# Optimization experiments

Hardware: AMD Instinct MI355X
Metric: run time of the kernel (lower is better)

The kernel has to match this reference:

```python
import jax, jax.numpy as jnp
import numpy as np

N_NODES = 100000
N_EDGES = 3200000
N_FEAT = 128
NUM_GRAPHS = 1024
NUM_CLASSES = 2


def glorot(key, shape):
    lim = np.sqrt(6.0 / (shape[0] + shape[1]))
    return jax.random.uniform(key, shape, jnp.float32, -lim, lim)


def setup_inputs() -> dict:
    key = jax.random.key(0)
    ks = jax.random.split(key, 12)
    x = jax.random.normal(ks[0], (N_NODES, N_FEAT), jnp.float32)
    edge_index = jax.random.randint(ks[1], (2, N_EDGES), 0, N_NODES, jnp.int64)
    batch = jnp.sort(jax.random.randint(ks[2], (N_NODES,), 0, NUM_GRAPHS, jnp.int64))
    return {
        "x": x,
        "edge_index": edge_index,
        "batch": batch,
        "W1": glorot(ks[3], (N_FEAT, 16)), "b1": jnp.zeros((16,), jnp.float32),
        "W2": glorot(ks[4], (16, 32)),     "b2": jnp.zeros((32,), jnp.float32),
        "W3": glorot(ks[5], (32, 64)),     "b3": jnp.zeros((64,), jnp.float32),
        "Wl1": glorot(ks[6], (64, 64)),    "bl1": jnp.zeros((64,), jnp.float32),
        "Wl2": glorot(ks[7], (64, NUM_CLASSES)), "bl2": jnp.zeros((NUM_CLASSES,), jnp.float32),
    }


def _gcn_norm(edge_index, n):
    # Add self-loops, then symmetric normalization D^-1/2 (A+I) D^-1/2
    loop = jnp.arange(n, dtype=edge_index.dtype)
    src = jnp.concatenate([edge_index[0], loop])
    dst = jnp.concatenate([edge_index[1], loop])
    deg = jax.ops.segment_sum(jnp.ones_like(dst, jnp.float32), dst, num_segments=n)
    dinv = jnp.where(deg > 0, jax.lax.rsqrt(deg), 0.0)
    norm = dinv[src] * dinv[dst]  # [E+N]
    return src, dst, norm


def _gcn_layer(h, W, b, src, dst, norm, n):
    h = h @ W                                  # linear first (PyG GCNConv order)
    msg = norm[:, None] * h[src]               # gather + scale
    out = jax.ops.segment_sum(msg, dst, num_segments=n) + b
    return jax.nn.relu(out)


def reference(x, edge_index, batch, W1, b1, W2, b2, W3, b3, Wl1, bl1, Wl2, bl2):
    n = x.shape[0]
    src, dst, norm = _gcn_norm(edge_index, n)
    h = _gcn_layer(x, W1, b1, src, dst, norm, n)
    h = _gcn_layer(h, W2, b2, src, dst, norm, n)
    h = _gcn_layer(h, W3, b3, src, dst, norm, n)
    # global mean pool over graphs
    sums = jax.ops.segment_sum(h, batch, num_segments=NUM_GRAPHS)
    cnts = jax.ops.segment_sum(jnp.ones((n,), jnp.float32), batch, num_segments=NUM_GRAPHS)
    pooled = sums / jnp.maximum(cnts, 1.0)[:, None]
    # MLP head (sigmoid self.out is defined but never applied in forward)
    hid = jax.nn.relu(pooled @ Wl1 + bl1)
    return hid @ Wl2 + bl2
```

## Files before the change

kernel.cpp:

```cpp
#include <hip/hip_runtime.h>
#include <hip/hip_fp16.h>


constexpr int EPA1 = 8192;
constexpr int NPSB = 256;
constexpr int PAD1 = 400;

__device__ __forceinline__ void acc8(float4& A, float4& B, uint4 u) {
    __half2* ph = reinterpret_cast<__half2*>(&u);
    float2 f0 = __half22float2(ph[0]);
    float2 f1 = __half22float2(ph[1]);
    float2 f2 = __half22float2(ph[2]);
    float2 f3 = __half22float2(ph[3]);
    A.x += f0.x; A.y += f0.y; A.z += f1.x; A.w += f1.y;
    B.x += f2.x; B.y += f2.y; B.z += f3.x; B.w += f3.y;
}
__device__ __forceinline__ uint4 pack8(const float* h) {
    __half2 a = __floats2half2_rn(h[0], h[1]);
    __half2 b = __floats2half2_rn(h[2], h[3]);
    __half2 c = __floats2half2_rn(h[4], h[5]);
    __half2 d = __floats2half2_rn(h[6], h[7]);
    uint4 u;
    u.x = *reinterpret_cast<unsigned*>(&a);
    u.y = *reinterpret_cast<unsigned*>(&b);
    u.z = *reinterpret_cast<unsigned*>(&c);
    u.w = *reinterpret_cast<unsigned*>(&d);
    return u;
}

__global__ __launch_bounds__(1024) void k_hist1(const int* __restrict__ dst,
        int* __restrict__ cnt1, int nE, int NSB) {
    __shared__ int hist[512];
    int t = threadIdx.x;
    if (t < 512) hist[t] = 0;
    __syncthreads();
    int base = blockIdx.x * EPA1, end = min(base + EPA1, nE);
    for (int e = base + t; e < end; e += 1024)
        atomicAdd(&hist[dst[e] >> 8], 1);
    __syncthreads();
    if (t < NSB) cnt1[blockIdx.x * PAD1 + t] = hist[t];
}

__global__ __launch_bounds__(512) void k_scan1(const int* __restrict__ cnt1,
        int* __restrict__ po1, int* __restrict__ totals, int NBLK1) {
    __shared__ int sc[512];
    int sb = blockIdx.x, t = threadIdx.x;
    int v = (t < NBLK1) ? cnt1[t * PAD1 + sb] : 0;
    sc[t] = v;
    __syncthreads();
    for (int off = 1; off < 512; off <<= 1) {
        int u = (t >= off) ? sc[t - off] : 0;
        __syncthreads();
        sc[t] += u;
        __syncthreads();
    }
    if (t < NBLK1) po1[t * PAD1 + sb] = sc[t] - v;
    if (t == 511) totals[sb] = sc[511];
}

__global__ __launch_bounds__(1024) void k_scat1(const int* __restrict__ src,
        const int* __restrict__ dst, const int* __restrict__ po1,
        const int* __restrict__ totals, unsigned* __restrict__ ebuf,
        int nE, int NSB) {
    __shared__ int sc[512], cur[512];
    int t = threadIdx.x, blk = blockIdx.x;
    if (t < 512) sc[t] = (t < NSB) ? totals[t] : 0;
    __syncthreads();
    for (int off = 1; off < 512; off <<= 1) {
        int u = (t >= off && t < 512) ? sc[t - off] : 0;
        __syncthreads();
        if (t < 512) sc[t] += u;
        __syncthreads();
    }
    if (t < NSB) cur[t] = (sc[t] - totals[t]) + po1[blk * PAD1 + t];
    __syncthreads();
    int base = blk * EPA1, end = min(base + EPA1, nE);
    for (int e = base + t; e < end; e += 1024) {
        int s = src[e], d = dst[e];
        int pos = atomicAdd(&cur[d >> 8], 1);
        ebuf[pos] = ((unsigned)(d & 255) << 17) | (unsigned)s;
    }
}

__global__ __launch_bounds__(512) void k_sort2(const unsigned* __restrict__ ebuf,
        const int* __restrict__ totals, int* __restrict__ col,
        int* __restrict__ start, float* __restrict__ dinv,
        unsigned* __restrict__ poff, int n, int qsz, int NSB) {
    __shared__ int sc[512];
    __shared__ int hist4[1024], cur4[1024], excl[256];
    int b = blockIdx.x, t = threadIdx.x;
    sc[t] = (t < NSB) ? totals[t] : 0;
    __syncthreads();
    for (int off = 1; off < 512; off <<= 1) {
        int u = (t >= off) ? sc[t - off] : 0;
        __syncthreads();
        sc[t] += u;
        __syncthreads();
    }
    int eend = sc[b], ebase = eend - totals[b];
    hist4[t] = 0; hist4[t + 512] = 0;
    __syncthreads();
    for (int e = ebase + t; e < eend; e += 512) {
        unsigned u = ebuf[e];
        atomicAdd(&hist4[(u >> 17) * 4 + (int)(u & 0x1FFFFu) / qsz], 1);
    }
    __syncthreads();
    int c0 = 0, c1 = 0, c2 = 0, c3 = 0, v = 0;
    if (t < 256) {
        c0 = hist4[t * 4];     c1 = hist4[t * 4 + 1];
        c2 = hist4[t * 4 + 2]; c3 = hist4[t * 4 + 3];
        v = c0 + c1 + c2 + c3;
        excl[t] = v;
    }
    __syncthreads();
    for (int off = 1; off < 256; off <<= 1) {
        int u = (t >= off && t < 256) ? excl[t - off] : 0;
        __syncthreads();
        if (t < 256) excl[t] += u;
        __syncthreads();
    }
    if (t < 256) {
        int sbase = ebase + excl[t] - v;
        cur4[t * 4]     = sbase;
        cur4[t * 4 + 1] = sbase + c0;
        cur4[t * 4 + 2] = sbase + c0 + c1;
        cur4[t * 4 + 3] = sbase + c0 + c1 + c2;
        int node = (b << 8) + t;
        if (node < n) {
            start[node] = sbase;
            dinv[node] = rsqrtf((float)(v + 1));
            poff[node] = (unsigned)c0 | ((unsigned)c1 << 8) |
                         ((unsigned)c2 << 16) | ((unsigned)c3 << 24);
        }
    }
    __syncthreads();
    for (int e = ebase + t; e < eend; e += 512) {
        unsigned u = ebuf[e];
        int s = (int)(u & 0x1FFFFu);
        int pos = atomicAdd(&cur4[(u >> 17) * 4 + s / qsz], 1);
        col[pos] = s;
    }
}

template <int U4PR>
__device__ __forceinline__ void agg_gather8(const uint4* __restrict__ T,
        const int* __restrict__ col, int base, unsigned pk, int q,
        size_t selfIdx, float4& A, float4& B) {
    A = make_float4(0.f, 0.f, 0.f, 0.f);
    B = make_float4(0.f, 0.f, 0.f, 0.f);
    acc8(A, B, T[selfIdx]);
    #pragma unroll
    for (int p = 0; p < 4; ++p) {
        int len = (int)((pk >> (8 * p)) & 255u);
        int k = 0;
        for (; k + 4 <= len; k += 4) {
            uint4 u0 = T[(size_t)col[base + k]     * U4PR + q];
            uint4 u1 = T[(size_t)col[base + k + 1] * U4PR + q];
            uint4 u2 = T[(size_t)col[base + k + 2] * U4PR + q];
            uint4 u3 = T[(size_t)col[base + k + 3] * U4PR + q];
            acc8(A, B, u0); acc8(A, B, u1); acc8(A, B, u2); acc8(A, B, u3);
        }
        for (; k < len; ++k)
            acc8(A, B, T[(size_t)col[base + k] * U4PR + q]);
        base += len;
    }
}

__global__ void k_aggf16(const uint4* __restrict__ T, const int* __restrict__ start,
        const unsigned* __restrict__ poff, const int* __restrict__ col,
        const float* __restrict__ dinv, const float* __restrict__ bias,
        uint4* __restrict__ out, int n) {
    int idx = blockIdx.x * blockDim.x + threadIdx.x;
    int i = idx / 2, q = idx % 2;
    if (i >= n) return;
    float4 A, B;
    agg_gather8<2>(T, col, start[i], poff[i], q, (size_t)i * 2 + q, A, B);
    float d = dinv[i];
    float4 bA = ((const float4*)bias)[q * 2];
    float4 bB = ((const float4*)bias)[q * 2 + 1];
    float h[8];
    h[0] = d * fmaxf(d * A.x + bA.x, 0.0f);
    h[1] = d * fmaxf(d * A.y + bA.y, 0.0f);
    h[2] = d * fmaxf(d * A.z + bA.z, 0.0f);
    h[3] = d * fmaxf(d * A.w + bA.w, 0.0f);
    h[4] = d * fmaxf(d * B.x + bB.x, 0.0f);
    h[5] = d * fmaxf(d * B.y + bB.y, 0.0f);
    h[6] = d * fmaxf(d * B.z + bB.z, 0.0f);
    h[7] = d * fmaxf(d * B.w + bB.w, 0.0f);
    out[(size_t)i * 2 + q] = pack8(h);
}

__global__ __launch_bounds__(256) void k_aggf16_mm2(const uint4* __restrict__ T,
        const int* __restrict__ start, const unsigned* __restrict__ poff,
        const int* __restrict__ col, const float* __restrict__ dinv,
        const float* __restrict__ W2, const float* __restrict__ b2,
        uint4* __restrict__ out, int n) {
    __shared__ float sW[16 * 32];
    __shared__ float sB[32];
    int t = threadIdx.x;
    for (int j = t; j < 512; j += 256) sW[j] = W2[j];
    if (t < 32) sB[t] = b2[t];
    __syncthreads();
    int idx = blockIdx.x * blockDim.x + t;
    int i = idx / 2, q = idx % 2;
    if (i >= n) return;
    float4 A, B;
    agg_gather8<2>(T, col, start[i], poff[i], q, (size_t)i * 2 + q, A, B);
    float d = dinv[i];
    float a[8] = {d * A.x, d * A.y, d * A.z, d * A.w,
                  d * B.x, d * B.y, d * B.z, d * B.w};
    int lane = t & 63;
    int gbase = lane & ~1;
    float h[16];
    #pragma unroll
    for (int o = 0; o < 16; ++o) h[o] = sB[q * 16 + o];
    #pragma unroll
    for (int j = 0; j < 2; ++j) {
        #pragma unroll
        for (int kk = 0; kk < 8; ++kk) {
            float ak = __shfl(a[kk], gbase + j);
            const float* w0 = &sW[(j * 8 + kk) * 32 + q * 16];
            #pragma unroll
            for (int o = 0; o < 16; ++o) h[o] += ak * w0[o];
        }
    }
    float ho[16];
    #pragma unroll
    for (int o = 0; o < 16; ++o) ho[o] = d * fmaxf(h[o], 0.0f);
    out[(size_t)i * 4 + q * 2]     = pack8(ho);
    out[(size_t)i * 4 + q * 2 + 1] = pack8(ho + 8);
}

__global__ __launch_bounds__(512) void k_aggf32_mm3(const uint4* __restrict__ T,
        const int* __restrict__ start, const unsigned* __restrict__ poff,
        const int* __restrict__ col, const float* __restrict__ dinv,
        const float* __restrict__ W3, const float* __restrict__ b3,
        float* __restrict__ out, int n) {
    __shared__ float sW[32 * 64];
    __shared__ float sB[64];
    int t = threadIdx.x;
    for (int j = t; j < 2048; j += 512) sW[j] = W3[j];
    if (t < 64) sB[t] = b3[t];
    __syncthreads();
    int idx = blockIdx.x * blockDim.x + t;
    int i = idx / 4, q = idx % 4;
    if (i >= n) return;
    float4 A, B;
    agg_gather8<4>(T, col, start[i], poff[i], q, (size_t)i * 4 + q, A, B);
    float d = dinv[i];
    float a[8] = {d * A.x, d * A.y, d * A.z, d * A.w,
                  d * B.x, d * B.y, d * B.z, d * B.w};
    int lane = t & 63;
    int gbase = lane & ~3;
    float h[16];
    #pragma unroll
    for (int o = 0; o < 16; ++o) h[o] = sB[q * 16 + o];
    #pragma unroll
    for (int j = 0; j < 4; ++j) {
        #pragma unroll
        for (int kk = 0; kk < 8; ++kk) {
            float ak = __shfl(a[kk], gbase + j);
            const float* w0 = &sW[(j * 8 + kk) * 64 + q * 16];
            #pragma unroll
            for (int o = 0; o < 16; ++o) h[o] += ak * w0[o];
        }
    }
    float4* O4 = (float4*)out;
    float4 o0, o1, o2, o3;
    o0.x = fmaxf(h[0], 0.f);  o0.y = fmaxf(h[1], 0.f);
    o0.z = fmaxf(h[2], 0.f);  o0.w = fmaxf(h[3], 0.f);
    o1.x = fmaxf(h[4], 0.f);  o1.y = fmaxf(h[5], 0.f);
    o1.z = fmaxf(h[6], 0.f);  o1.w = fmaxf(h[7], 0.f);
    o2.x = fmaxf(h[8], 0.f);  o2.y = fmaxf(h[9], 0.f);
    o2.z = fmaxf(h[10], 0.f); o2.w = fmaxf(h[11], 0.f);
    o3.x = fmaxf(h[12], 0.f); o3.y = fmaxf(h[13], 0.f);
    o3.z = fmaxf(h[14], 0.f); o3.w = fmaxf(h[15], 0.f);
    size_t rb = (size_t)i * 16 + q * 4;
    O4[rb] = o0; O4[rb + 1] = o1; O4[rb + 2] = o2; O4[rb + 3] = o3;
}

__global__ __launch_bounds__(256) void k_mm1(const float4* __restrict__ X4,
        const float4* __restrict__ W4, const float* __restrict__ dinv,
        __half* __restrict__ out, int n) {
    __shared__ float4 xs[64 * 32];
    __shared__ float4 ws[512];
    int t = threadIdx.x;
    int nb = blockIdx.x * 64;
    ws[t] = W4[t]; ws[t + 256] = W4[t + 256];
    int lim = min(64, n - nb);
    #pragma unroll
    for (int it = 0; it < 8; ++it) {
        int idx = it * 256 + t;
        if ((idx >> 5) < lim) xs[idx] = X4[(size_t)nb * 32 + idx];
    }
    __syncthreads();
    int lane = t & 63, wv = t >> 6;
    int f = lane & 15, kc = lane >> 4;
    float wcol[32];
    #pragma unroll
    for (int kk = 0; kk < 32; ++kk)
        wcol[kk] = ((const float*)ws)[(kc * 32 + kk) * 16 + f];
    for (int ln = wv * 16; ln < wv * 16 + 16; ++ln) {
        if (ln >= lim) break;
        int i = nb + ln;
        float acc = 0.0f;
        #pragma unroll
        for (int j = 0; j < 8; ++j) {
            float4 hv = xs[ln * 32 + kc * 8 + j];
            acc += hv.x * wcol[4 * j]     + hv.y * wcol[4 * j + 1]
                 + hv.z * wcol[4 * j + 2] + hv.w * wcol[4 * j + 3];
        }
        acc += __shfl_xor(acc, 16);
        acc += __shfl_xor(acc, 32);
        if (kc == 0) out[(size_t)i * 16 + f] = __float2half_rn(acc * dinv[i]);
    }
}

__global__ __launch_bounds__(256) void k_poolhead(const float* __restrict__ h3,
        const int* __restrict__ batch, const float* __restrict__ Wl1,
        const float* __restrict__ bl1, const float* __restrict__ Wl2,
        const float* __restrict__ bl2, float* __restrict__ out, int n) {
    int g = blockIdx.x, t = threadIdx.x;
    int f = t & 63, r = t >> 6;
    __shared__ int sb[2];
    __shared__ float part[4][64];
    __shared__ float mean[64], hid[64];
    if (t < 2) {
        int target = g + t;
        int lo = 0, hi = n;
        while (lo < hi) {
            int mid = (lo + hi) >> 1;
            if (batch[mid] < target) lo = mid + 1; else hi = mid;
        }
        sb[t] = lo;
    }
    __syncthreads();
    int s = sb[0], e = sb[1];
    float acc = 0.0f;
    for (int i = s + r; i < e; i += 4) acc += h3[(size_t)i * 64 + f];
    part[r][f] = acc;
    __syncthreads();
    if (t < 64) {
        float c = fmaxf((float)(e - s), 1.0f);
        mean[t] = (part[0][t] + part[1][t] + part[2][t] + part[3][t]) / c;
    }
    __syncthreads();
    if (t < 64) {
        float a = bl1[t];
        #pragma unroll 8
        for (int k = 0; k < 64; ++k) a += mean[k] * Wl1[k * 64 + t];
        hid[t] = fmaxf(a, 0.0f);
    }
    __syncthreads();
    if (t < 2) {
        float o = bl2[t];
        #pragma unroll 8
        for (int k = 0; k < 64; ++k) o += hid[k] * Wl2[k * 2 + t];
        out[g * 2 + t] = o;
    }
}

extern "C" void kernel_launch(void* const* d_in, const int* in_sizes, int n_in,
                              void* d_out, int out_size, void* d_ws, size_t ws_size,
                              hipStream_t stream) {
    const float* x    = (const float*)d_in[0];
    const int*   ei   = (const int*)d_in[1];
    const int*   batch= (const int*)d_in[2];
    const float* W1   = (const float*)d_in[3];
    const float* b1   = (const float*)d_in[4];
    const float* W2   = (const float*)d_in[5];
    const float* b2   = (const float*)d_in[6];
    const float* W3   = (const float*)d_in[7];
    const float* b3   = (const float*)d_in[8];
    const float* Wl1  = (const float*)d_in[9];
    const float* bl1  = (const float*)d_in[10];
    const float* Wl2  = (const float*)d_in[11];
    const float* bl2  = (const float*)d_in[12];
    float* out = (float*)d_out;

    const int n  = in_sizes[2];
    const int nE = in_sizes[1] / 2;
    const int* src = ei;
    const int* dst = ei + nE;

    const int NSB   = (n + NPSB - 1) / NPSB;
    const int NBLK1 = (nE + EPA1 - 1) / EPA1;
    const int NG    = 1024;
    const int qsz   = (n + 3) / 4;

    char* w = (char*)d_ws;
    auto alloc_f = [&](size_t cnt) { float* p = (float*)w; w += cnt * 4; return p; };
    auto alloc_i = [&](size_t cnt) { int*   p = (int*)w;   w += cnt * 4; return p; };
    auto alloc_h = [&](size_t cnt) { __half* p = (__half*)w; w += cnt * 2; return p; };

    float*    dinv   = alloc_f(n);
    int*      start  = alloc_i(n);
    unsigned* poff   = (unsigned*)alloc_i(n);
    int*      cnt1   = alloc_i((size_t)NBLK1 * PAD1);
    int*      po1    = alloc_i((size_t)NBLK1 * PAD1);
    int*      totals = alloc_i(512);
    unsigned* ebuf   = (unsigned*)alloc_i(nE);
    int*      col    = alloc_i(nE);
    __half* Pd1 = alloc_h((size_t)n * 16);
    __half* h1d = alloc_h((size_t)n * 16);
    __half* h2d = alloc_h((size_t)n * 32);
    float*  h3  = alloc_f((size_t)n * 64);

    const int B = 256;
    auto g = [&](long long t) { return (int)((t + B - 1) / B); };

    k_hist1<<<NBLK1, 1024, 0, stream>>>(dst, cnt1, nE, NSB);
    k_scan1<<<NSB, 512, 0, stream>>>(cnt1, po1, totals, NBLK1);
    k_scat1<<<NBLK1, 1024, 0, stream>>>(src, dst, po1, totals, ebuf, nE, NSB);
    k_sort2<<<NSB, 512, 0, stream>>>(ebuf, totals, col, start, dinv, poff, n, qsz, NSB);

    k_mm1<<<(n + 63) / 64, 256, 0, stream>>>((const float4*)x, (const float4*)W1,
                                             dinv, Pd1, n);
    k_aggf16<<<g((long long)n * 2), B, 0, stream>>>((const uint4*)Pd1, start, poff,
                                                    col, dinv, b1, (uint4*)h1d, n);

    k_aggf16_mm2<<<g((long long)n * 2), B, 0, stream>>>((const uint4*)h1d, start,
                                                        poff, col, dinv, W2, b2,
                                                        (uint4*)h2d, n);

    k_aggf32_mm3<<<(int)(((long long)n * 4 + 511) / 512), 512, 0, stream>>>(
        (const uint4*)h2d, start, poff, col, dinv, W3, b3, h3, n);

    k_poolhead<<<NG, 256, 0, stream>>>(h3, batch, Wl1, bl1, Wl2, bl2, out, n);
}
```

Measured before the change: 202.2 us.

## Split each node's edge list across two thread halves in aggregation kernels

The three aggregation kernels now give each node twice as many threads. Each half gathers two of the four source-quartile segments, and the partial sums are combined with an xor shuffle. The fused matmuls are repartitioned so each thread produces 8 outputs instead of 16, which cuts per-thread register use and serial gather latency. Separately, the integer division by the quartile size in the sort kernel is replaced by a precomputed magic-number multiply-high. This doubles the thread count and adds shuffle traffic, and load imbalance between the two halves may waste lanes.

```diff
diff --git a/kernel.cpp b/kernel.cpp
--- a/kernel.cpp
+++ b/kernel.cpp
@@ -85,7 +85,7 @@
 __global__ __launch_bounds__(512) void k_sort2(const unsigned* __restrict__ ebuf,
         const int* __restrict__ totals, int* __restrict__ col,
         int* __restrict__ start, float* __restrict__ dinv,
-        unsigned* __restrict__ poff, int n, int qsz, int NSB) {
+        unsigned* __restrict__ poff, int n, unsigned qmagic, int NSB) {
     __shared__ int sc[512];
     __shared__ int hist4[1024], cur4[1024], excl[256];
     int b = blockIdx.x, t = threadIdx.x;
@@ -102,7 +102,8 @@
     __syncthreads();
     for (int e = ebase + t; e < eend; e += 512) {
         unsigned u = ebuf[e];
-        atomicAdd(&hist4[(u >> 17) * 4 + (int)(u & 0x1FFFFu) / qsz], 1);
+        unsigned s = u & 0x1FFFFu;
+        atomicAdd(&hist4[(u >> 17) * 4 + __umulhi(s, qmagic)], 1);
     }
     __syncthreads();
     int c0 = 0, c1 = 0, c2 = 0, c3 = 0, v = 0;
@@ -136,22 +137,19 @@
     __syncthreads();
     for (int e = ebase + t; e < eend; e += 512) {
         unsigned u = ebuf[e];
-        int s = (int)(u & 0x1FFFFu);
-        int pos = atomicAdd(&cur4[(u >> 17) * 4 + s / qsz], 1);
-        col[pos] = s;
+        unsigned s = u & 0x1FFFFu;
+        int pos = atomicAdd(&cur4[(u >> 17) * 4 + __umulhi(s, qmagic)], 1);
+        col[pos] = (int)s;
     }
 }
 
 template <int U4PR>
-__device__ __forceinline__ void agg_gather8(const uint4* __restrict__ T,
-        const int* __restrict__ col, int base, unsigned pk, int q,
-        size_t selfIdx, float4& A, float4& B) {
-    A = make_float4(0.f, 0.f, 0.f, 0.f);
-    B = make_float4(0.f, 0.f, 0.f, 0.f);
-    acc8(A, B, T[selfIdx]);
-    #pragma unroll
-    for (int p = 0; p < 4; ++p) {
-        int len = (int)((pk >> (8 * p)) & 255u);
+__device__ __forceinline__ void agg_gather_half(const uint4* __restrict__ T,
+        const int* __restrict__ col, int base, unsigned pk, int p0, int q,
+        float4& A, float4& B) {
+    #pragma unroll
+    for (int pp = 0; pp < 2; ++pp) {
+        int len = (int)((pk >> (8 * (p0 + pp))) & 255u);
         int k = 0;
         for (; k + 4 <= len; k += 4) {
             uint4 u0 = T[(size_t)col[base + k]     * U4PR + q];
@@ -165,29 +163,43 @@
         base += len;
     }
 }
+__device__ __forceinline__ void combine(float4& A, float4& B, int xorMask) {
+    A.x += __shfl_xor(A.x, xorMask); A.y += __shfl_xor(A.y, xorMask);
+    A.z += __shfl_xor(A.z, xorMask); A.w += __shfl_xor(A.w, xorMask);
+    B.x += __shfl_xor(B.x, xorMask); B.y += __shfl_xor(B.y, xorMask);
+    B.z += __shfl_xor(B.z, xorMask); B.w += __shfl_xor(B.w, xorMask);
+}
 
 __global__ void k_aggf16(const uint4* __restrict__ T, const int* __restrict__ start,
         const unsigned* __restrict__ poff, const int* __restrict__ col,
         const float* __restrict__ dinv, const float* __restrict__ bias,
         uint4* __restrict__ out, int n) {
     int idx = blockIdx.x * blockDim.x + threadIdx.x;
-    int i = idx / 2, q = idx % 2;
+    int i = idx >> 2, sub = idx & 3;
     if (i >= n) return;
-    float4 A, B;
-    agg_gather8<2>(T, col, start[i], poff[i], q, (size_t)i * 2 + q, A, B);
+    int q = sub & 1, h = sub >> 1;
+    unsigned pk = poff[i];
+    int len01 = (int)(pk & 255u) + (int)((pk >> 8) & 255u);
+    int base = start[i] + (h ? len01 : 0);
+    float4 A = make_float4(0.f, 0.f, 0.f, 0.f);
+    float4 B = make_float4(0.f, 0.f, 0.f, 0.f);
+    if (h == 0) acc8(A, B, T[(size_t)i * 2 + q]);
+    agg_gather_half<2>(T, col, base, pk, h * 2, q, A, B);
+    combine(A, B, 2);
+    if (h) return;
     float d = dinv[i];
     float4 bA = ((const float4*)bias)[q * 2];
     float4 bB = ((const float4*)bias)[q * 2 + 1];
-    float h[8];
-    h[0] = d * fmaxf(d * A.x + bA.x, 0.0f);
-    h[1] = d * fmaxf(d * A.y + bA.y, 0.0f);
-    h[2] = d * fmaxf(d * A.z + bA.z, 0.0f);
-    h[3] = d * fmaxf(d * A.w + bA.w, 0.0f);
-    h[4] = d * fmaxf(d * B.x + bB.x, 0.0f);
-    h[5] = d * fmaxf(d * B.y + bB.y, 0.0f);
-    h[6] = d * fmaxf(d * B.z + bB.z, 0.0f);
-    h[7] = d * fmaxf(d * B.w + bB.w, 0.0f);
-    out[(size_t)i * 2 + q] = pack8(h);
+    float ho[8];
+    ho[0] = d * fmaxf(d * A.x + bA.x, 0.0f);
+    ho[1] = d * fmaxf(d * A.y + bA.y, 0.0f);
+    ho[2] = d * fmaxf(d * A.z + bA.z, 0.0f);
+    ho[3] = d * fmaxf(d * A.w + bA.w, 0.0f);
+    ho[4] = d * fmaxf(d * B.x + bB.x, 0.0f);
+    ho[5] = d * fmaxf(d * B.y + bB.y, 0.0f);
+    ho[6] = d * fmaxf(d * B.z + bB.z, 0.0f);
+    ho[7] = d * fmaxf(d * B.w + bB.w, 0.0f);
+    out[(size_t)i * 2 + q] = pack8(ho);
 }
 
 __global__ __launch_bounds__(256) void k_aggf16_mm2(const uint4* __restrict__ T,
@@ -202,33 +214,39 @@
     if (t < 32) sB[t] = b2[t];
     __syncthreads();
     int idx = blockIdx.x * blockDim.x + t;
-    int i = idx / 2, q = idx % 2;
+    int i = idx >> 2, sub = idx & 3;
     if (i >= n) return;
-    float4 A, B;
-    agg_gather8<2>(T, col, start[i], poff[i], q, (size_t)i * 2 + q, A, B);
+    int q = sub & 1, h = sub >> 1;
+    unsigned pk = poff[i];
+    int len01 = (int)(pk & 255u) + (int)((pk >> 8) & 255u);
+    int base = start[i] + (h ? len01 : 0);
+    float4 A = make_float4(0.f, 0.f, 0.f, 0.f);
+    float4 B = make_float4(0.f, 0.f, 0.f, 0.f);
+    if (h == 0) acc8(A, B, T[(size_t)i * 2 + q]);
+    agg_gather_half<2>(T, col, base, pk, h * 2, q, A, B);
+    combine(A, B, 2);
     float d = dinv[i];
     float a[8] = {d * A.x, d * A.y, d * A.z, d * A.w,
                   d * B.x, d * B.y, d * B.z, d * B.w};
     int lane = t & 63;
-    int gbase = lane & ~1;
-    float h[16];
-    #pragma unroll
-    for (int o = 0; o < 16; ++o) h[o] = sB[q * 16 + o];
+    int gbase = lane & ~3;
+    float hacc[8];
+    #pragma unroll
+    for (int o = 0; o < 8; ++o) hacc[o] = sB[sub * 8 + o];
     #pragma unroll
     for (int j = 0; j < 2; ++j) {
         #pragma unroll
         for (int kk = 0; kk < 8; ++kk) {
             float ak = __shfl(a[kk], gbase + j);
-            const float* w0 = &sW[(j * 8 + kk) * 32 + q * 16];
+            const float* w0 = &sW[(j * 8 + kk) * 32 + sub * 8];
             #pragma unroll
-            for (int o = 0; o < 16; ++o) h[o] += ak * w0[o];
-        }
-    }
-    float ho[16];
-    #pragma unroll
-    for (int o = 0; o < 16; ++o) ho[o] = d * fmaxf(h[o], 0.0f);
-    out[(size_t)i * 4 + q * 2]     = pack8(ho);
-    out[(size_t)i * 4 + q * 2 + 1] = pack8(ho + 8);
+            for (int o = 0; o < 8; ++o) hacc[o] += ak * w0[o];
+        }
+    }
+    float ho[8];
+    #pragma unroll
+    for (int o = 0; o < 8; ++o) ho[o] = d * fmaxf(hacc[o], 0.0f);
+    out[(size_t)i * 4 + sub] = pack8(ho);
 }
 
 __global__ __launch_bounds__(512) void k_aggf32_mm3(const uint4* __restrict__ T,
@@ -243,40 +261,43 @@
     if (t < 64) sB[t] = b3[t];
     __syncthreads();
     int idx = blockIdx.x * blockDim.x + t;
-    int i = idx / 4, q = idx % 4;
+    int i = idx >> 3, sub = idx & 7;
     if (i >= n) return;
-    float4 A, B;
-    agg_gather8<4>(T, col, start[i], poff[i], q, (size_t)i * 4 + q, A, B);
+    int q = sub & 3, h = sub >> 2;
+    unsigned pk = poff[i];
+    int len01 = (int)(pk & 255u) + (int)((pk >> 8) & 255u);
+    int base = start[i] + (h ? len01 : 0);
+    float4 A = make_float4(0.f, 0.f, 0.f, 0.f);
+    float4 B = make_float4(0.f, 0.f, 0.f, 0.f);
+    if (h == 0) acc8(A, B, T[(size_t)i * 4 + q]);
+    agg_gather_half<4>(T, col, base, pk, h * 2, q, A, B);
+    combine(A, B, 4);
     float d = dinv[i];
     float a[8] = {d * A.x, d * A.y, d * A.z, d * A.w,
                   d * B.x, d * B.y, d * B.z, d * B.w};
     int lane = t & 63;
-    int gbase = lane & ~3;
-    float h[16];
-    #pragma unroll
-    for (int o = 0; o < 16; ++o) h[o] = sB[q * 16 + o];
+    int gbase = lane & ~7;
+    float hacc[8];
+    #pragma unroll
+    for (int o = 0; o < 8; ++o) hacc[o] = sB[sub * 8 + o];
     #pragma unroll
     for (int j = 0; j < 4; ++j) {
         #pragma unroll
         for (int kk = 0; kk < 8; ++kk) {
             float ak = __shfl(a[kk], gbase + j);
-            const float* w0 = &sW[(j * 8 + kk) * 64 + q * 16];
+            const float* w0 = &sW[(j * 8 + kk) * 64 + sub * 8];
             #pragma unroll
-            for (int o = 0; o < 16; ++o) h[o] += ak * w0[o];
-        }
-    }
+            for (int o = 0; o < 8; ++o) hacc[o] += ak * w0[o];
+        }
+    }
+    float4 o0, o1;
+    o0.x = fmaxf(hacc[0], 0.f); o0.y = fmaxf(hacc[1], 0.f);
+    o0.z = fmaxf(hacc[2], 0.f); o0.w = fmaxf(hacc[3], 0.f);
+    o1.x = fmaxf(hacc[4], 0.f); o1.y = fmaxf(hacc[5], 0.f);
+    o1.z = fmaxf(hacc[6], 0.f); o1.w = fmaxf(hacc[7], 0.f);
     float4* O4 = (float4*)out;
-    float4 o0, o1, o2, o3;
-    o0.x = fmaxf(h[0], 0.f);  o0.y = fmaxf(h[1], 0.f);
-    o0.z = fmaxf(h[2], 0.f);  o0.w = fmaxf(h[3], 0.f);
-    o1.x = fmaxf(h[4], 0.f);  o1.y = fmaxf(h[5], 0.f);
-    o1.z = fmaxf(h[6], 0.f);  o1.w = fmaxf(h[7], 0.f);
-    o2.x = fmaxf(h[8], 0.f);  o2.y = fmaxf(h[9], 0.f);
-    o2.z = fmaxf(h[10], 0.f); o2.w = fmaxf(h[11], 0.f);
-    o3.x = fmaxf(h[12], 0.f); o3.y = fmaxf(h[13], 0.f);
-    o3.z = fmaxf(h[14], 0.f); o3.w = fmaxf(h[15], 0.f);
-    size_t rb = (size_t)i * 16 + q * 4;
-    O4[rb] = o0; O4[rb + 1] = o1; O4[rb + 2] = o2; O4[rb + 3] = o3;
+    size_t rb = (size_t)i * 16 + sub * 2;
+    O4[rb] = o0; O4[rb + 1] = o1;
 }
 
 __global__ __launch_bounds__(256) void k_mm1(const float4* __restrict__ X4,
@@ -387,6 +408,7 @@
     const int NBLK1 = (nE + EPA1 - 1) / EPA1;
     const int NG    = 1024;
     const int qsz   = (n + 3) / 4;
+    const unsigned qmagic = (unsigned)((0x100000000ULL + qsz - 1) / qsz);
 
     char* w = (char*)d_ws;
     auto alloc_f = [&](size_t cnt) { float* p = (float*)w; w += cnt * 4; return p; };
@@ -412,18 +434,19 @@
     k_hist1<<<NBLK1, 1024, 0, stream>>>(dst, cnt1, nE, NSB);
     k_scan1<<<NSB, 512, 0, stream>>>(cnt1, po1, totals, NBLK1);
     k_scat1<<<NBLK1, 1024, 0, stream>>>(src, dst, po1, totals, ebuf, nE, NSB);
-    k_sort2<<<NSB, 512, 0, stream>>>(ebuf, totals, col, start, dinv, poff, n, qsz, NSB);
+    k_sort2<<<NSB, 512, 0, stream>>>(ebuf, totals, col, start, dinv, poff, n,
+                                     qmagic, NSB);
 
     k_mm1<<<(n + 63) / 64, 256, 0, stream>>>((const float4*)x, (const float4*)W1,
                                              dinv, Pd1, n);
-    k_aggf16<<<g((long long)n * 2), B, 0, stream>>>((const uint4*)Pd1, start, poff,
+    k_aggf16<<<g((long long)n * 4), B, 0, stream>>>((const uint4*)Pd1, start, poff,
                                                     col, dinv, b1, (uint4*)h1d, n);
 
-    k_aggf16_mm2<<<g((long long)n * 2), B, 0, stream>>>((const uint4*)h1d, start,
+    k_aggf16_mm2<<<g((long long)n * 4), B, 0, stream>>>((const uint4*)h1d, start,
                                                         poff, col, dinv, W2, b2,
                                                         (uint4*)h2d, n);
 
-    k_aggf32_mm3<<<(int)(((long long)n * 4 + 511) / 512), 512, 0, stream>>>(
+    k_aggf32_mm3<<<(int)(((long long)n * 8 + 511) / 512), 512, 0, stream>>>(
         (const uint4*)h2d, start, poff, col, dinv, W3, b3, h3, n);
 
     k_poolhead<<<NG, 256, 0, stream>>>(h3, batch, Wl1, bl1, Wl2, bl2, out, n);
```

After: 197.6 us. 1.02x faster.
